# Kernel tuning notes

Measured on AMD Instinct MI355X. Metric: run time of the kernel, lower is better.

The kernel has to match this reference:

```python
import jax, jax.numpy as jnp
import numpy as np

# ---- maxflat pyramid filters (pfilters('maxflat')) ----
def _maxflat_filters():
    sqrt2 = np.sqrt(2.0)
    M1 = M2 = 1.0 / sqrt2
    k1 = 1.0 - sqrt2
    k2 = k3 = M1
    h_half = np.array([0.25 * k2 * k3, 0.5 * k2, 1.0 + 0.5 * k2 * k3]) * M1
    h = np.concatenate([h_half, h_half[:-1][::-1]]) * sqrt2          # len 5
    g_half = np.array([-0.125 * k1 * k2 * k3,
                       0.25 * k1 * k2,
                       -0.5 * k1 - 0.5 * k3 - 0.375 * k1 * k2 * k3,
                       1.0 + 0.5 * k1 * k2]) * M2
    g = np.concatenate([g_half, g_half[:-1][::-1]]) * sqrt2          # len 7
    return h.astype(np.float32), g.astype(np.float32)

# highpass from g, as in wfb2dec: h1 = -g * (-1)**(arange(1,L+1)-c)
def _wfb_filters():
    h, g = _maxflat_filters()
    len_h1 = len(g)                      # 7 (odd)
    c = int(np.floor((len_h1 + 1.0) / 2.0))   # 4
    h1 = (-g * (-1.0) ** (np.arange(1, len_h1 + 1) - c)).astype(np.float32)
    ext_h0 = int(np.floor(len(h) / 2.0))      # 2
    ext_h1 = len_h1 - c + 1                   # 4
    return h, h1, ext_h0, ext_h1

# periodic row filtering along last axis (torch rowfiltering: periodic pad +
# cross-correlation, which F.conv2d / lax conv both compute without flip)
def rowfilt(x, f, ext1):
    L = f.shape[0]
    ext2 = L - ext1 - 1
    W = x.shape[-1]
    xe = jnp.concatenate([x[..., -ext1:], x, x[..., :ext2]], axis=-1)
    y = f[0] * xe[..., 0:W]
    for k in range(1, L):                 # tiny fixed tap loop, fuses fine
        y = y + f[k] * xe[..., k:k + W]
    return y

def colfilt(x, f, ext1):
    return jnp.swapaxes(rowfilt(jnp.swapaxes(x, -1, -2), f, ext1), -1, -2)


def setup_inputs() -> dict:
    key = jax.random.key(0)
    x = jax.random.normal(key, (8, 3, 1024, 1024), dtype=jnp.float32)
    return {"x": x}


def reference(x):
    # Pycontourlet.batch_multi_channel_pdfbdec with pfilt='maxflat',
    # nlevs=[0] -> wfb2dec path: one level of separable wavelet FB with
    # periodic extension; returns [xLL, [xLH, xHL, xHH]] (stacked here).
    h_np, h1_np, e0, e1 = _wfb_filters()
    h = jnp.asarray(h_np)
    h1 = jnp.asarray(h1_np)

    x_L = rowfilt(x, h, e0)[..., ::2]          # [B,C,H,W/2]
    x_H = rowfilt(x, h1, e1)[..., ::2]

    x_LL = colfilt(x_L, h, e0)[..., ::2, :]    # [B,C,H/2,W/2]
    x_LH = colfilt(x_L, h1, e1)[..., ::2, :]
    x_HL = colfilt(x_H, h, e0)[..., ::2, :]
    x_HH = colfilt(x_H, h1, e1)[..., ::2, :]

    return jnp.stack([x_LL, x_LH, x_HL, x_HH])  # [4,B,C,H/2,W/2]
```

## Files before the change

### kernel.cpp

```cpp
#include <hip/hip_runtime.h>


constexpr int H = 1024, W = 1024;
constexpr int NIMG = 24;
constexpr int HOUT = 512, WOUT = 512;
constexpr int TO = 32;
constexpr int NT = 4;
constexpr int RIN = 69;
constexpr int PAD = 36;
constexpr int NITEM = RIN * 4;

__global__ __launch_bounds__(256, 4)
void wfb_kernel(const float* __restrict__ x, float* __restrict__ out) {
    __shared__ float s_L[2][RIN][PAD];
    __shared__ float s_H[2][RIN][PAD];

    const float h0c[5] = {0.125f, 0.35355339059327373f, 1.25f,
                          0.35355339059327373f, 0.125f};
    const float h1c[7] = {0.025888347648318447f,  0.07322330470336313f,
                          -0.06878156646177083f, -0.8535533905932737f,
                          -0.06878156646177083f,  0.07322330470336313f,
                          0.025888347648318447f};

    const int tid = threadIdx.x;
    const int img = blockIdx.z;
    const int r0 = blockIdx.y * TO;
    const int c0b = blockIdx.x * (NT * TO);
    const float* __restrict__ xin = x + (size_t)img * H * W;
    const int rbase = 2 * r0 - 4;

    const int m0 = tid;
    const int m1 = tid + 256;
    const bool has1 = (m1 < NITEM);
    const int r_0 = m0 >> 2, g_0 = m0 & 3;
    const int r_1 = (has1 ? m1 : m0) >> 2, g_1 = (has1 ? m1 : m0) & 3;
    const float* __restrict__ rowp0 = xin + (size_t)((rbase + r_0) & (H - 1)) * W;
    const float* __restrict__ rowp1 = xin + (size_t)((rbase + r_1) & (H - 1)) * W;

    float v0[24], v1[24];

    auto LOAD = [&](int t) {
        const int cbase = 2 * (c0b + t * TO) - 4;
        {
            const int b0 = cbase + 16 * g_0;
            #pragma unroll
            for (int q = 0; q < 6; ++q) {
                int gc = (b0 + 4 * q) & (W - 1);
                float4 f = *(const float4*)(rowp0 + gc);
                v0[4*q+0] = f.x; v0[4*q+1] = f.y;
                v0[4*q+2] = f.z; v0[4*q+3] = f.w;
            }
        }
        if (has1) {
            const int b0 = cbase + 16 * g_1;
            #pragma unroll
            for (int q = 0; q < 6; ++q) {
                int gc = (b0 + 4 * q) & (W - 1);
                float4 f = *(const float4*)(rowp1 + gc);
                v1[4*q+0] = f.x; v1[4*q+1] = f.y;
                v1[4*q+2] = f.z; v1[4*q+3] = f.w;
            }
        }
    };

    auto ROWFILT = [&](int buf) {
        {
            float Lo[8], Ho[8];
            #pragma unroll
            for (int u = 0; u < 8; ++u) {
                const float* p = v0 + 2 * u;
                Lo[u] = h0c[0]*p[2] + h0c[1]*p[3] + h0c[2]*p[4]
                      + h0c[3]*p[5] + h0c[4]*p[6];
                Ho[u] = h1c[0]*p[0] + h1c[1]*p[1] + h1c[2]*p[2] + h1c[3]*p[3]
                      + h1c[4]*p[4] + h1c[5]*p[5] + h1c[6]*p[6];
            }
            const int j0 = 8 * g_0;
            *(float4*)&s_L[buf][r_0][j0]     = make_float4(Lo[0],Lo[1],Lo[2],Lo[3]);
            *(float4*)&s_L[buf][r_0][j0 + 4] = make_float4(Lo[4],Lo[5],Lo[6],Lo[7]);
            *(float4*)&s_H[buf][r_0][j0]     = make_float4(Ho[0],Ho[1],Ho[2],Ho[3]);
            *(float4*)&s_H[buf][r_0][j0 + 4] = make_float4(Ho[4],Ho[5],Ho[6],Ho[7]);
        }
        if (has1) {
            float Lo[8], Ho[8];
            #pragma unroll
            for (int u = 0; u < 8; ++u) {
                const float* p = v1 + 2 * u;
                Lo[u] = h0c[0]*p[2] + h0c[1]*p[3] + h0c[2]*p[4]
                      + h0c[3]*p[5] + h0c[4]*p[6];
                Ho[u] = h1c[0]*p[0] + h1c[1]*p[1] + h1c[2]*p[2] + h1c[3]*p[3]
                      + h1c[4]*p[4] + h1c[5]*p[5] + h1c[6]*p[6];
            }
            const int j0 = 8 * g_1;
            *(float4*)&s_L[buf][r_1][j0]     = make_float4(Lo[0],Lo[1],Lo[2],Lo[3]);
            *(float4*)&s_L[buf][r_1][j0 + 4] = make_float4(Lo[4],Lo[5],Lo[6],Lo[7]);
            *(float4*)&s_H[buf][r_1][j0]     = make_float4(Ho[0],Ho[1],Ho[2],Ho[3]);
            *(float4*)&s_H[buf][r_1][j0 + 4] = make_float4(Ho[4],Ho[5],Ho[6],Ho[7]);
        }
    };

    constexpr size_t SB = (size_t)NIMG * HOUT * WOUT;
    float* __restrict__ o = out + (size_t)img * HOUT * WOUT;
    const int i_  = tid >> 3;
    const int jj_ = (tid & 7) * 4;

    auto PHASE2 = [&](int t) {
        const int buf = t & 1;
        const int c0 = c0b + t * TO;
        float LLx=0,LLy=0,LLz=0,LLw=0, HLx=0,HLy=0,HLz=0,HLw=0;
        float LHx=0,LHy=0,LHz=0,LHw=0, HHx=0,HHy=0,HHz=0,HHw=0;
        #pragma unroll
        for (int k = 0; k < 5; ++k) {
            float4 a = *(const float4*)&s_L[buf][2*i_ + 2 + k][jj_];
            float4 b = *(const float4*)&s_H[buf][2*i_ + 2 + k][jj_];
            LLx += h0c[k]*a.x; LLy += h0c[k]*a.y; LLz += h0c[k]*a.z; LLw += h0c[k]*a.w;
            HLx += h0c[k]*b.x; HLy += h0c[k]*b.y; HLz += h0c[k]*b.z; HLw += h0c[k]*b.w;
        }
        #pragma unroll
        for (int k = 0; k < 7; ++k) {
            float4 a = *(const float4*)&s_L[buf][2*i_ + k][jj_];
            float4 b = *(const float4*)&s_H[buf][2*i_ + k][jj_];
            LHx += h1c[k]*a.x; LHy += h1c[k]*a.y; LHz += h1c[k]*a.z; LHw += h1c[k]*a.w;
            HHx += h1c[k]*b.x; HHy += h1c[k]*b.y; HHz += h1c[k]*b.z; HHw += h1c[k]*b.w;
        }
        size_t off = (size_t)(r0 + i_) * WOUT + (c0 + jj_);
        *(float4*)(o + 0 * SB + off) = make_float4(LLx, LLy, LLz, LLw);
        *(float4*)(o + 1 * SB + off) = make_float4(LHx, LHy, LHz, LHw);
        *(float4*)(o + 2 * SB + off) = make_float4(HLx, HLy, HLz, HLw);
        *(float4*)(o + 3 * SB + off) = make_float4(HHx, HHy, HHz, HHw);
    };

    LOAD(0);
    ROWFILT(0);
    LOAD(1);
    __syncthreads();

    #pragma unroll
    for (int t = 0; t < NT; ++t) {
        if (t + 1 < NT) ROWFILT((t + 1) & 1);
        if (t + 2 < NT) LOAD(t + 2);
        PHASE2(t);
        if (t + 1 < NT) __syncthreads();
    }
}

extern "C" void kernel_launch(void* const* d_in, const int* in_sizes, int n_in,
                              void* d_out, int out_size, void* d_ws, size_t ws_size,
                              hipStream_t stream) {
    const float* x = (const float*)d_in[0];
    float* out = (float*)d_out;
    dim3 grid(WOUT / (TO * NT), HOUT / TO, NIMG);
    wfb_kernel<<<grid, dim3(256), 0, stream>>>(x, out);
}
```

Before: 189.8 us.

## Single-buffer LDS tiles, halve tiles per block, raise occupancy target

Replaces the double-buffered shared-memory tiles with a single buffer and adds a second barrier so the row-filter stage writes only after the column stage has consumed the tile. Each block now handles two column tiles instead of four, doubling the grid, and launch bounds ask for eight blocks per CU instead of four. The aim is to cut LDS and register use per block so more waves stay resident and hide global-memory latency, at the cost of losing the overlap between row filtering and column filtering and recomputing more halo per output.

```diff
diff --git a/kernel.cpp b/kernel.cpp
--- a/kernel.cpp
+++ b/kernel.cpp
@@ -5,15 +5,15 @@
 constexpr int NIMG = 24;
 constexpr int HOUT = 512, WOUT = 512;
 constexpr int TO = 32;
-constexpr int NT = 4;
+constexpr int NT = 2;
 constexpr int RIN = 69;
 constexpr int PAD = 36;
 constexpr int NITEM = RIN * 4;
 
-__global__ __launch_bounds__(256, 4)
+__global__ __launch_bounds__(256, 8)
 void wfb_kernel(const float* __restrict__ x, float* __restrict__ out) {
-    __shared__ float s_L[2][RIN][PAD];
-    __shared__ float s_H[2][RIN][PAD];
+    __shared__ float s_L[RIN][PAD];
+    __shared__ float s_H[RIN][PAD];
 
     const float h0c[5] = {0.125f, 0.35355339059327373f, 1.25f,
                           0.35355339059327373f, 0.125f};
@@ -63,7 +63,7 @@
         }
     };
 
-    auto ROWFILT = [&](int buf) {
+    auto ROWFILT = [&]() {
         {
             float Lo[8], Ho[8];
             #pragma unroll
@@ -75,10 +75,10 @@
                       + h1c[4]*p[4] + h1c[5]*p[5] + h1c[6]*p[6];
             }
             const int j0 = 8 * g_0;
-            *(float4*)&s_L[buf][r_0][j0]     = make_float4(Lo[0],Lo[1],Lo[2],Lo[3]);
-            *(float4*)&s_L[buf][r_0][j0 + 4] = make_float4(Lo[4],Lo[5],Lo[6],Lo[7]);
-            *(float4*)&s_H[buf][r_0][j0]     = make_float4(Ho[0],Ho[1],Ho[2],Ho[3]);
-            *(float4*)&s_H[buf][r_0][j0 + 4] = make_float4(Ho[4],Ho[5],Ho[6],Ho[7]);
+            *(float4*)&s_L[r_0][j0]     = make_float4(Lo[0],Lo[1],Lo[2],Lo[3]);
+            *(float4*)&s_L[r_0][j0 + 4] = make_float4(Lo[4],Lo[5],Lo[6],Lo[7]);
+            *(float4*)&s_H[r_0][j0]     = make_float4(Ho[0],Ho[1],Ho[2],Ho[3]);
+            *(float4*)&s_H[r_0][j0 + 4] = make_float4(Ho[4],Ho[5],Ho[6],Ho[7]);
         }
         if (has1) {
             float Lo[8], Ho[8];
@@ -91,10 +91,10 @@
                       + h1c[4]*p[4] + h1c[5]*p[5] + h1c[6]*p[6];
             }
             const int j0 = 8 * g_1;
-            *(float4*)&s_L[buf][r_1][j0]     = make_float4(Lo[0],Lo[1],Lo[2],Lo[3]);
-            *(float4*)&s_L[buf][r_1][j0 + 4] = make_float4(Lo[4],Lo[5],Lo[6],Lo[7]);
-            *(float4*)&s_H[buf][r_1][j0]     = make_float4(Ho[0],Ho[1],Ho[2],Ho[3]);
-            *(float4*)&s_H[buf][r_1][j0 + 4] = make_float4(Ho[4],Ho[5],Ho[6],Ho[7]);
+            *(float4*)&s_L[r_1][j0]     = make_float4(Lo[0],Lo[1],Lo[2],Lo[3]);
+            *(float4*)&s_L[r_1][j0 + 4] = make_float4(Lo[4],Lo[5],Lo[6],Lo[7]);
+            *(float4*)&s_H[r_1][j0]     = make_float4(Ho[0],Ho[1],Ho[2],Ho[3]);
+            *(float4*)&s_H[r_1][j0 + 4] = make_float4(Ho[4],Ho[5],Ho[6],Ho[7]);
         }
     };
 
@@ -104,21 +104,20 @@
     const int jj_ = (tid & 7) * 4;
 
     auto PHASE2 = [&](int t) {
-        const int buf = t & 1;
         const int c0 = c0b + t * TO;
         float LLx=0,LLy=0,LLz=0,LLw=0, HLx=0,HLy=0,HLz=0,HLw=0;
         float LHx=0,LHy=0,LHz=0,LHw=0, HHx=0,HHy=0,HHz=0,HHw=0;
         #pragma unroll
         for (int k = 0; k < 5; ++k) {
-            float4 a = *(const float4*)&s_L[buf][2*i_ + 2 + k][jj_];
-            float4 b = *(const float4*)&s_H[buf][2*i_ + 2 + k][jj_];
+            float4 a = *(const float4*)&s_L[2*i_ + 2 + k][jj_];
+            float4 b = *(const float4*)&s_H[2*i_ + 2 + k][jj_];
             LLx += h0c[k]*a.x; LLy += h0c[k]*a.y; LLz += h0c[k]*a.z; LLw += h0c[k]*a.w;
             HLx += h0c[k]*b.x; HLy += h0c[k]*b.y; HLz += h0c[k]*b.z; HLw += h0c[k]*b.w;
         }
         #pragma unroll
         for (int k = 0; k < 7; ++k) {
-            float4 a = *(const float4*)&s_L[buf][2*i_ + k][jj_];
-            float4 b = *(const float4*)&s_H[buf][2*i_ + k][jj_];
+            float4 a = *(const float4*)&s_L[2*i_ + k][jj_];
+            float4 b = *(const float4*)&s_H[2*i_ + k][jj_];
             LHx += h1c[k]*a.x; LHy += h1c[k]*a.y; LHz += h1c[k]*a.z; LHw += h1c[k]*a.w;
             HHx += h1c[k]*b.x; HHy += h1c[k]*b.y; HHz += h1c[k]*b.z; HHw += h1c[k]*b.w;
         }
@@ -130,16 +129,19 @@
     };
 
     LOAD(0);
-    ROWFILT(0);
+    ROWFILT();
     LOAD(1);
     __syncthreads();
 
     #pragma unroll
     for (int t = 0; t < NT; ++t) {
-        if (t + 1 < NT) ROWFILT((t + 1) & 1);
-        if (t + 2 < NT) LOAD(t + 2);
         PHASE2(t);
-        if (t + 1 < NT) __syncthreads();
+        if (t + 1 < NT) {
+            __syncthreads();
+            ROWFILT();
+            if (t + 2 < NT) LOAD(t + 2);
+            __syncthreads();
+        }
     }
 }
 
```

After: 210.5 us. 1.11x slower.
